# Optimization experiments

Measured on AMD Instinct MI355X. Metric: run time of the kernel, lower is better.

## Reference

```python
import jax, jax.numpy as jnp
import numpy as np

N = 4096
REG_STRENGTH = 1.0
BLOCK_EPS = 1e-6  # tolerance for detecting pooled-block boundaries in the backward


@jax.custom_vjp
def isotonic_l2(y):
    """argmin_{v_1 >= v_2 >= ... >= v_n} 0.5 * ||v - y||^2 (PAV solution).

    Computed via the exact minimax characterization, fully vectorized:
        v_i = min_{j <= i} max_{k >= i} mean(y[j..k])
    """
    return _iso_solution(y)


def _iso_solution(y):
    n = y.shape[0]
    cs = jnp.concatenate([jnp.zeros((1,), y.dtype), jnp.cumsum(y)])  # [n+1]
    idx = jnp.arange(n)
    j = idx[:, None]  # block start
    k = idx[None, :]  # block end
    length = (k - j + 1).astype(y.dtype)
    A = (cs[k + 1] - cs[j]) / length            # mean(y[j..k]) where k >= j
    A = jnp.where(k >= j, A, -jnp.inf)
    # M[j, i] = max_{k >= i} A[j, k]  (reverse cumulative max along k)
    M = jnp.flip(jax.lax.cummax(jnp.flip(A, axis=1), axis=1), axis=1)
    # v_i = min_{j <= i} M[j, i]  (cumulative min along j, take diagonal)
    v = jnp.diagonal(jax.lax.cummin(M, axis=0))
    return v


def _iso_fwd(y):
    v = _iso_solution(y)
    return v, v


def _iso_bwd(v, g):
    # Jacobian of PAV: within each pooled block, grad is the block mean of g.
    n = v.shape[0]
    drop = (v[:-1] - v[1:]) > BLOCK_EPS * jnp.maximum(jnp.abs(v[:-1]), 1.0)
    bid = jnp.concatenate([jnp.zeros((1,), jnp.int32),
                           jnp.cumsum(drop.astype(jnp.int32))])
    sums = jax.ops.segment_sum(g, bid, num_segments=n)
    cnts = jax.ops.segment_sum(jnp.ones_like(g), bid, num_segments=n)
    return ((sums / jnp.maximum(cnts, 1.0))[bid],)


isotonic_l2.defvjp(_iso_fwd, _iso_bwd)


def soft_rank(x, regularization_strength):
    """torchsort-style L2 soft rank: project x/eps onto permutahedron P([n..1])."""
    n = x.shape[0]
    theta = x / regularization_strength
    perm = jnp.argsort(-theta)          # descending sort permutation (constant wrt grad)
    s = theta[perm]
    w = jnp.arange(n, 0, -1, dtype=x.dtype)  # [n, n-1, ..., 1]
    sol = isotonic_l2(s - w)
    ranks_sorted = s - sol
    inv = jnp.argsort(perm)
    return ranks_sorted[inv]


def setup_inputs() -> dict:
    key = jax.random.key(0)
    kp, kt = jax.random.split(key)
    pred = jax.random.normal(kp, (N,), dtype=jnp.float32)
    target = jax.random.normal(kt, (N,), dtype=jnp.float32)
    return {"pred": pred, "target": target}


def reference(pred, target):
    p = soft_rank(pred, REG_STRENGTH)
    t = soft_rank(target, REG_STRENGTH)
    p = p - p.mean()
    p = p / jnp.linalg.norm(p)
    t = t - t.mean()
    t = t / jnp.linalg.norm(t)
    return 1.0 - jnp.sum(p * t)
```

## Files before the change

kernel.cpp:

```cpp
#include <hip/hip_runtime.h>
#include <math.h>

#define NEL   4096
#define NT    1024
#define HALF  512
#define EPT   8
#define CPT   4
#define CB    256

#define IX(p) ((p) + ((p) >> 3))

#define WSYNC() asm volatile("s_waitcnt lgkmcnt(0)" ::: "memory")

__global__ __launch_bounds__(CB)
void count_kernel(const float* __restrict__ pred,
                  const float* __restrict__ target,
                  unsigned int* __restrict__ counts) {
  __shared__ float jv[CB];
  const int arr = blockIdx.z;
  const float* __restrict__ x = arr ? target : pred;
  const int i     = blockIdx.x * CB + threadIdx.x;
  const int jbase = blockIdx.y * CB;

  jv[threadIdx.x] = x[jbase + threadIdx.x];
  const float xi = x[i];
  __syncthreads();

  const float4* jv4 = (const float4*)jv;
  unsigned int c = 0;
#pragma unroll 4
  for (int t4 = 0; t4 < CB / 4; t4++) {
    const float4 v = jv4[t4];
    const int j = jbase + 4 * t4;
    c += (v.x > xi || (v.x == xi && j + 0 < i)) ? 1u : 0u;
    c += (v.y > xi || (v.y == xi && j + 1 < i)) ? 1u : 0u;
    c += (v.z > xi || (v.z == xi && j + 2 < i)) ? 1u : 0u;
    c += (v.w > xi || (v.w == xi && j + 3 < i)) ? 1u : 0u;
  }
  atomicAdd(&counts[arr * NEL + i], c);
}

__device__ inline void pav_merge(double* P, int* C, const int lo, const int mid,
                                 const int hi) {
  const int llen = C[mid - 1];
  int cs = mid - llen;
  const int rlen = C[mid];
  int ce = mid + rlen - 1;
  const double Pmid = P[IX(mid)];
  double Pcs = P[IX(cs)], Pce1 = P[IX(ce + 1)];
  if ((Pmid - Pcs) * (double)rlen <= (Pce1 - Pmid) * (double)llen) {
    bool changed = true;
    while (changed) {
      changed = false;
      while (cs > lo) {
        const int l2 = C[cs - 1];
        const double Pl = P[IX(cs - l2)];
        if ((Pcs - Pl) * (double)(ce - cs + 1) <= (Pce1 - Pcs) * (double)l2) {
          cs -= l2; Pcs = Pl; changed = true;
        } else break;
      }
      while (ce < hi - 1) {
        const int l2 = C[ce + 1];
        const double Pr = P[IX(ce + 1 + l2)];
        if ((Pr - Pce1) * (double)(ce - cs + 1) >= (Pce1 - Pcs) * (double)l2) {
          ce += l2; Pce1 = Pr; changed = true;
        } else break;
      }
    }
    const int len = ce - cs + 1;
    C[cs] = len;
    C[ce] = len;
  }
}

__global__ __launch_bounds__(NT)
void pav_loss_kernel(const float* __restrict__ pred,
                     const float* __restrict__ target,
                     const unsigned int* __restrict__ counts,
                     float* __restrict__ loss_out) {
  __shared__ float  s_val[2][IX(NEL - 1) + 2];
  __shared__ double s_P[2][IX(NEL) + 1];
  __shared__ int    s_cnt[2][NEL];
  __shared__ double s_wsum[2][HALF / 64];
  __shared__ int    s_nb[2];
  __shared__ double s_red[NT / 64][5];

  const int tid  = threadIdx.x;
  const int lane = tid & 63;
  const int wid  = tid >> 6;

  int rp[CPT], rt[CPT];
  {
    const uint4 a = ((const uint4*)counts)[tid];
    const uint4 b = ((const uint4*)counts)[NEL / 4 + tid];
    rp[0] = (int)a.x; rp[1] = (int)a.y; rp[2] = (int)a.z; rp[3] = (int)a.w;
    rt[0] = (int)b.x; rt[1] = (int)b.y; rt[2] = (int)b.z; rt[3] = (int)b.w;
    const float4 xp = ((const float4*)pred)[tid];
    const float4 xt = ((const float4*)target)[tid];
    s_val[0][IX(rp[0])] = xp.x; s_val[0][IX(rp[1])] = xp.y;
    s_val[0][IX(rp[2])] = xp.z; s_val[0][IX(rp[3])] = xp.w;
    s_val[1][IX(rt[0])] = xt.x; s_val[1][IX(rt[1])] = xt.y;
    s_val[1][IX(rt[2])] = xt.z; s_val[1][IX(rt[3])] = xt.w;
  }
  __syncthreads();

  const int arr = tid >> 9;
  const int tA  = tid & (HALF - 1);
  const int wA  = tA >> 6;
  const int b0  = tA * EPT;
  double* P = s_P[arr];
  int*    C = s_cnt[arr];

  double c[EPT];
  {
    double acc = 0.0;
#pragma unroll
    for (int e = 0; e < EPT; e++) {
      const int p = b0 + e;
      acc += (double)s_val[arr][IX(p)] - (double)(NEL - p);
      c[e] = acc;
    }
  }
  const double tot = c[EPT - 1];
  double sc = tot;
#pragma unroll
  for (int d = 1; d < 64; d <<= 1) {
    const double o = __shfl_up(sc, d, 64);
    if (lane >= d) sc += o;
  }
  if (lane == 63) s_wsum[arr][wA] = sc;
  __syncthreads();
  double wexcl = 0.0;
#pragma unroll
  for (int w = 0; w < HALF / 64; w++)
    wexcl += (w < wA) ? s_wsum[arr][w] : 0.0;
  const double excl = wexcl + (sc - tot);
#pragma unroll
  for (int e = 0; e < EPT; e++) P[IX(b0 + 1 + e)] = excl + c[e];
  if (lane == 0) P[IX(b0)] = excl;

  double nmx[EPT]; int dmx[EPT];
  double vn[EPT];  int vd[EPT];
  {
#pragma unroll
    for (int j = 0; j < EPT; j++) {
      nmx[j] = c[7] - (j ? c[j - 1] : 0.0);
      dmx[j] = EPT - j;
    }
    double mn = nmx[0]; int md = dmx[0];
#pragma unroll
    for (int j = 1; j < EPT; j++)
      if (nmx[j] * (double)md < mn * (double)dmx[j]) { mn = nmx[j]; md = dmx[j]; }
    vn[7] = mn; vd[7] = md;
#pragma unroll
    for (int p = EPT - 2; p >= 0; p--) {
#pragma unroll
      for (int j = 0; j < EPT - 1; j++) {
        if (j <= p) {
          const double cnum = c[p] - (j ? c[j - 1] : 0.0);
          const int cden = p - j + 1;
          if (cnum * (double)dmx[j] > nmx[j] * (double)cden) {
            nmx[j] = cnum; dmx[j] = cden;
          }
        }
      }
      double mn2 = nmx[0]; int md2 = dmx[0];
#pragma unroll
      for (int j = 1; j < EPT - 1; j++) {
        if (j <= p) {
          if (nmx[j] * (double)md2 < mn2 * (double)dmx[j]) {
            mn2 = nmx[j]; md2 = dmx[j];
          }
        }
      }
      vn[p] = mn2; vd[p] = md2;
    }
  }
  {
    int runstart = b0;
#pragma unroll
    for (int e = 1; e < EPT; e++) {
      const bool neq = (vd[e] != vd[e - 1]) ||
                       (__double_as_longlong(vn[e]) !=
                        __double_as_longlong(vn[e - 1]));
      if (neq) {
        const int len = b0 + e - runstart;
        C[runstart] = len;
        C[b0 + e - 1] = len;
        runstart = b0 + e;
      }
    }
    const int len = b0 + EPT - runstart;
    C[runstart] = len;
    C[b0 + EPT - 1] = len;
  }
  WSYNC();

  const int wbase = wA * 512;
#pragma unroll
  for (int m = EPT; m <= 256; m <<= 1) {
    const int nm = 512 / (2 * m);
    if (lane < nm) {
      const int lo = wbase + lane * 2 * m;
      pav_merge(P, C, lo, lo + m, lo + 2 * m);
    }
    WSYNC();
  }
  __syncthreads();

  if (wA == 0) {
#pragma unroll
    for (int m = 512; m <= 2048; m <<= 1) {
      const int nm = NEL / (2 * m);
      if (lane < nm) {
        const int lo = lane * 2 * m;
        pav_merge(P, C, lo, lo + m, lo + 2 * m);
      }
      WSYNC();
    }
    if (lane == 0) {
      int s = 0, b = 0;
      while (s < NEL) {
        const int cc = C[s];
        C[b] = s;
        b++;
        s += cc;
      }
      s_nb[arr] = b;
    }
  }
  __syncthreads();

  const int nb = s_nb[arr];
#pragma unroll
  for (int e = 0; e < EPT; e++) {
    const int p = b0 + e;
    int lo = 0, hi = nb - 1;
    while (lo < hi) {
      const int md = (lo + hi + 1) >> 1;
      if (C[md] <= p) lo = md; else hi = md - 1;
    }
    const int st = C[lo];
    const int en = (lo + 1 < nb) ? C[lo + 1] : NEL;
    const double v = (P[IX(en)] - P[IX(st)]) / (double)(en - st);
    s_val[arr][IX(p)] = (float)((double)s_val[arr][IX(p)] - v);
  }
  __syncthreads();

  double Sp = 0.0, Sq = 0.0, Spp = 0.0, Sqq = 0.0, Spq = 0.0;
#pragma unroll
  for (int e = 0; e < CPT; e++) {
    const double p = (double)s_val[0][IX(rp[e])];
    const double q = (double)s_val[1][IX(rt[e])];
    Sp += p; Sq += q; Spp += p * p; Sqq += q * q; Spq += p * q;
  }
#pragma unroll
  for (int d = 32; d > 0; d >>= 1) {
    Sp  += __shfl_down(Sp,  d, 64);
    Sq  += __shfl_down(Sq,  d, 64);
    Spp += __shfl_down(Spp, d, 64);
    Sqq += __shfl_down(Sqq, d, 64);
    Spq += __shfl_down(Spq, d, 64);
  }
  if (lane == 0) {
    s_red[wid][0] = Sp;  s_red[wid][1] = Sq;  s_red[wid][2] = Spp;
    s_red[wid][3] = Sqq; s_red[wid][4] = Spq;
  }
  __syncthreads();
  if (tid == 0) {
    double a0 = 0, a1 = 0, a2 = 0, a3 = 0, a4 = 0;
    for (int w = 0; w < NT / 64; w++) {
      a0 += s_red[w][0]; a1 += s_red[w][1]; a2 += s_red[w][2];
      a3 += s_red[w][3]; a4 += s_red[w][4];
    }
    const double n  = (double)NEL;
    const double mp = a0 / n, mq = a1 / n;
    const double cov = a4 - n * mp * mq;
    const double vp  = a2 - n * mp * mp;
    const double vq  = a3 - n * mq * mq;
    loss_out[0] = (float)(1.0 - cov / sqrt(vp * vq));
  }
}

extern "C" void kernel_launch(void* const* d_in, const int* in_sizes, int n_in,
                              void* d_out, int out_size, void* d_ws, size_t ws_size,
                              hipStream_t stream) {
  const float* pred   = (const float*)d_in[0];
  const float* target = (const float*)d_in[1];
  unsigned int* counts = (unsigned int*)d_ws;
  float* out = (float*)d_out;

  hipMemsetAsync(counts, 0, 2 * NEL * sizeof(unsigned int), stream);
  hipLaunchKernelGGL(count_kernel, dim3(NEL / CB, NEL / CB, 2), dim3(CB), 0,
                     stream, pred, target, counts);
  hipLaunchKernelGGL(pav_loss_kernel, dim3(1), dim3(NT), 0, stream,
                     pred, target, counts, out);
}
```

Before: 80.52 us.

## Drop memset and atomics in rank count; scatter sorted values from count kernel

The counting kernel now has each block load the whole array into shared memory, and four lanes split the comparisons for one element and combine their partial counts with shuffles. This removes the memset, the global atomics and the 2D grid. The count kernel also scatters each value to its sorted position in a workspace buffer, so the single-block PAV kernel reads sorted values directly instead of scattering them through shared memory behind a barrier. The trade-off is fewer, longer-running count blocks (128 instead of 512) and extra workspace use.

```diff
diff --git a/kernel.cpp b/kernel.cpp
--- a/kernel.cpp
+++ b/kernel.cpp
@@ -6,38 +6,50 @@
 #define HALF  512
 #define EPT   8
 #define CPT   4
-#define CB    256
+#define LPI   4
+#define QPAD  1032
 
 #define IX(p) ((p) + ((p) >> 3))
 
 #define WSYNC() asm volatile("s_waitcnt lgkmcnt(0)" ::: "memory")
 
-__global__ __launch_bounds__(CB)
+__global__ __launch_bounds__(256)
 void count_kernel(const float* __restrict__ pred,
                   const float* __restrict__ target,
-                  unsigned int* __restrict__ counts) {
-  __shared__ float jv[CB];
-  const int arr = blockIdx.z;
+                  unsigned int* __restrict__ counts,
+                  float* __restrict__ sortedv) {
+  __shared__ float jv[4 * QPAD];
+  const int arr = blockIdx.y;
   const float* __restrict__ x = arr ? target : pred;
-  const int i     = blockIdx.x * CB + threadIdx.x;
-  const int jbase = blockIdx.y * CB;
-
-  jv[threadIdx.x] = x[jbase + threadIdx.x];
-  const float xi = x[i];
-  __syncthreads();
-
-  const float4* jv4 = (const float4*)jv;
+  const int tid = threadIdx.x;
+  const int q   = tid & (LPI - 1);
+  const int i   = blockIdx.x * 64 + (tid >> 2);
+
+  {
+    const float4* x4 = (const float4*)x;
+    for (int w4 = tid; w4 < NEL / 4; w4 += 256) {
+      const int qq = w4 >> 8;
+      ((float4*)(jv + qq * QPAD))[w4 & 255] = x4[w4];
+    }
+  }
+  __syncthreads();
+
+  const float xi = jv[(i >> 10) * QPAD + (i & 1023)];
+  const float4* mv = (const float4*)(jv + q * QPAD);
   unsigned int c = 0;
-#pragma unroll 4
-  for (int t4 = 0; t4 < CB / 4; t4++) {
-    const float4 v = jv4[t4];
-    const int j = jbase + 4 * t4;
+#pragma unroll 8
+  for (int t4 = 0; t4 < 256; t4++) {
+    const float4 v = mv[t4];
+    const int j = q * 1024 + 4 * t4;
     c += (v.x > xi || (v.x == xi && j + 0 < i)) ? 1u : 0u;
     c += (v.y > xi || (v.y == xi && j + 1 < i)) ? 1u : 0u;
     c += (v.z > xi || (v.z == xi && j + 2 < i)) ? 1u : 0u;
     c += (v.w > xi || (v.w == xi && j + 3 < i)) ? 1u : 0u;
   }
-  atomicAdd(&counts[arr * NEL + i], c);
+  c += __shfl_xor((int)c, 1);
+  c += __shfl_xor((int)c, 2);
+  if (q == 0) counts[arr * NEL + i] = c;
+  if (q == 1) sortedv[arr * NEL + c] = xi;
 }
 
 __device__ inline void pav_merge(double* P, int* C, const int lo, const int mid,
@@ -74,11 +86,10 @@
 }
 
 __global__ __launch_bounds__(NT)
-void pav_loss_kernel(const float* __restrict__ pred,
-                     const float* __restrict__ target,
-                     const unsigned int* __restrict__ counts,
+void pav_loss_kernel(const unsigned int* __restrict__ counts,
+                     const float* __restrict__ sortedv,
                      float* __restrict__ loss_out) {
-  __shared__ float  s_val[2][IX(NEL - 1) + 2];
+  __shared__ float  s_rank[2][IX(NEL - 1) + 1];
   __shared__ double s_P[2][IX(NEL) + 1];
   __shared__ int    s_cnt[2][NEL];
   __shared__ double s_wsum[2][HALF / 64];
@@ -95,14 +106,7 @@
     const uint4 b = ((const uint4*)counts)[NEL / 4 + tid];
     rp[0] = (int)a.x; rp[1] = (int)a.y; rp[2] = (int)a.z; rp[3] = (int)a.w;
     rt[0] = (int)b.x; rt[1] = (int)b.y; rt[2] = (int)b.z; rt[3] = (int)b.w;
-    const float4 xp = ((const float4*)pred)[tid];
-    const float4 xt = ((const float4*)target)[tid];
-    s_val[0][IX(rp[0])] = xp.x; s_val[0][IX(rp[1])] = xp.y;
-    s_val[0][IX(rp[2])] = xp.z; s_val[0][IX(rp[3])] = xp.w;
-    s_val[1][IX(rt[0])] = xt.x; s_val[1][IX(rt[1])] = xt.y;
-    s_val[1][IX(rt[2])] = xt.z; s_val[1][IX(rt[3])] = xt.w;
-  }
-  __syncthreads();
+  }
 
   const int arr = tid >> 9;
   const int tA  = tid & (HALF - 1);
@@ -111,13 +115,20 @@
   double* P = s_P[arr];
   int*    C = s_cnt[arr];
 
+  float xv[EPT];
+  {
+    const float4 v0 = ((const float4*)sortedv)[arr * (NEL / 4) + 2 * tA];
+    const float4 v1 = ((const float4*)sortedv)[arr * (NEL / 4) + 2 * tA + 1];
+    xv[0] = v0.x; xv[1] = v0.y; xv[2] = v0.z; xv[3] = v0.w;
+    xv[4] = v1.x; xv[5] = v1.y; xv[6] = v1.z; xv[7] = v1.w;
+  }
+
   double c[EPT];
   {
     double acc = 0.0;
 #pragma unroll
     for (int e = 0; e < EPT; e++) {
-      const int p = b0 + e;
-      acc += (double)s_val[arr][IX(p)] - (double)(NEL - p);
+      acc += (double)xv[e] - (double)(NEL - (b0 + e));
       c[e] = acc;
     }
   }
@@ -243,15 +254,15 @@
     const int st = C[lo];
     const int en = (lo + 1 < nb) ? C[lo + 1] : NEL;
     const double v = (P[IX(en)] - P[IX(st)]) / (double)(en - st);
-    s_val[arr][IX(p)] = (float)((double)s_val[arr][IX(p)] - v);
+    s_rank[arr][IX(p)] = (float)((double)xv[e] - v);
   }
   __syncthreads();
 
   double Sp = 0.0, Sq = 0.0, Spp = 0.0, Sqq = 0.0, Spq = 0.0;
 #pragma unroll
   for (int e = 0; e < CPT; e++) {
-    const double p = (double)s_val[0][IX(rp[e])];
-    const double q = (double)s_val[1][IX(rt[e])];
+    const double p = (double)s_rank[0][IX(rp[e])];
+    const double q = (double)s_rank[1][IX(rt[e])];
     Sp += p; Sq += q; Spp += p * p; Sqq += q * q; Spq += p * q;
   }
 #pragma unroll
@@ -287,12 +298,12 @@
                               hipStream_t stream) {
   const float* pred   = (const float*)d_in[0];
   const float* target = (const float*)d_in[1];
-  unsigned int* counts = (unsigned int*)d_ws;
+  unsigned int* counts  = (unsigned int*)d_ws;
+  float*        sortedv = (float*)((char*)d_ws + 2 * NEL * sizeof(unsigned int));
   float* out = (float*)d_out;
 
-  hipMemsetAsync(counts, 0, 2 * NEL * sizeof(unsigned int), stream);
-  hipLaunchKernelGGL(count_kernel, dim3(NEL / CB, NEL / CB, 2), dim3(CB), 0,
-                     stream, pred, target, counts);
+  hipLaunchKernelGGL(count_kernel, dim3(64, 2), dim3(256), 0, stream,
+                     pred, target, counts, sortedv);
   hipLaunchKernelGGL(pav_loss_kernel, dim3(1), dim3(NT), 0, stream,
-                     pred, target, counts, out);
+                     counts, sortedv, out);
 }
```

New measurement: 102.1 us. 1.27x slower.

## Halve PAV block threads, 16 elements each, with sequential stack-based local PAV

Applied to the files above, without the earlier changes.

Drops the PAV kernel from 1024 to 512 threads, each handling 16 sorted elements instead of 8. The unrolled minimax computation of each thread's local isotonic solution is replaced by a sequential pool-adjacent-violators loop over shared-memory prefix sums and block lengths. The in-wave merge tree now starts at 16 and covers 1024 elements per wave, so a single wave does fewer cross-wave merge levels. The trade-off is fewer threads sharing the work, a longer serial per-thread loop, and more shared-memory traffic in the local pass.

```diff
diff --git a/kernel.cpp b/kernel.cpp
--- a/kernel.cpp
+++ b/kernel.cpp
@@ -2,10 +2,10 @@
 #include <math.h>
 
 #define NEL   4096
-#define NT    1024
-#define HALF  512
-#define EPT   8
-#define CPT   4
+#define NT    512
+#define HALF  256
+#define EPT   16
+#define CPT   8
 #define CB    256
 
 #define IX(p) ((p) + ((p) >> 3))
@@ -91,20 +91,30 @@
 
   int rp[CPT], rt[CPT];
   {
-    const uint4 a = ((const uint4*)counts)[tid];
-    const uint4 b = ((const uint4*)counts)[NEL / 4 + tid];
-    rp[0] = (int)a.x; rp[1] = (int)a.y; rp[2] = (int)a.z; rp[3] = (int)a.w;
-    rt[0] = (int)b.x; rt[1] = (int)b.y; rt[2] = (int)b.z; rt[3] = (int)b.w;
-    const float4 xp = ((const float4*)pred)[tid];
-    const float4 xt = ((const float4*)target)[tid];
-    s_val[0][IX(rp[0])] = xp.x; s_val[0][IX(rp[1])] = xp.y;
-    s_val[0][IX(rp[2])] = xp.z; s_val[0][IX(rp[3])] = xp.w;
-    s_val[1][IX(rt[0])] = xt.x; s_val[1][IX(rt[1])] = xt.y;
-    s_val[1][IX(rt[2])] = xt.z; s_val[1][IX(rt[3])] = xt.w;
-  }
-  __syncthreads();
-
-  const int arr = tid >> 9;
+    const uint4 a0 = ((const uint4*)counts)[2 * tid];
+    const uint4 a1 = ((const uint4*)counts)[2 * tid + 1];
+    const uint4 b0_ = ((const uint4*)counts)[NEL / 4 + 2 * tid];
+    const uint4 b1_ = ((const uint4*)counts)[NEL / 4 + 2 * tid + 1];
+    rp[0] = (int)a0.x; rp[1] = (int)a0.y; rp[2] = (int)a0.z; rp[3] = (int)a0.w;
+    rp[4] = (int)a1.x; rp[5] = (int)a1.y; rp[6] = (int)a1.z; rp[7] = (int)a1.w;
+    rt[0] = (int)b0_.x; rt[1] = (int)b0_.y; rt[2] = (int)b0_.z; rt[3] = (int)b0_.w;
+    rt[4] = (int)b1_.x; rt[5] = (int)b1_.y; rt[6] = (int)b1_.z; rt[7] = (int)b1_.w;
+    const float4 xp0 = ((const float4*)pred)[2 * tid];
+    const float4 xp1 = ((const float4*)pred)[2 * tid + 1];
+    const float4 xt0 = ((const float4*)target)[2 * tid];
+    const float4 xt1 = ((const float4*)target)[2 * tid + 1];
+    s_val[0][IX(rp[0])] = xp0.x; s_val[0][IX(rp[1])] = xp0.y;
+    s_val[0][IX(rp[2])] = xp0.z; s_val[0][IX(rp[3])] = xp0.w;
+    s_val[0][IX(rp[4])] = xp1.x; s_val[0][IX(rp[5])] = xp1.y;
+    s_val[0][IX(rp[6])] = xp1.z; s_val[0][IX(rp[7])] = xp1.w;
+    s_val[1][IX(rt[0])] = xt0.x; s_val[1][IX(rt[1])] = xt0.y;
+    s_val[1][IX(rt[2])] = xt0.z; s_val[1][IX(rt[3])] = xt0.w;
+    s_val[1][IX(rt[4])] = xt1.x; s_val[1][IX(rt[5])] = xt1.y;
+    s_val[1][IX(rt[6])] = xt1.z; s_val[1][IX(rt[7])] = xt1.w;
+  }
+  __syncthreads();
+
+  const int arr = tid >> 8;
   const int tA  = tid & (HALF - 1);
   const int wA  = tA >> 6;
   const int b0  = tA * EPT;
@@ -139,67 +149,28 @@
   for (int e = 0; e < EPT; e++) P[IX(b0 + 1 + e)] = excl + c[e];
   if (lane == 0) P[IX(b0)] = excl;
 
-  double nmx[EPT]; int dmx[EPT];
-  double vn[EPT];  int vd[EPT];
-  {
-#pragma unroll
-    for (int j = 0; j < EPT; j++) {
-      nmx[j] = c[7] - (j ? c[j - 1] : 0.0);
-      dmx[j] = EPT - j;
-    }
-    double mn = nmx[0]; int md = dmx[0];
-#pragma unroll
-    for (int j = 1; j < EPT; j++)
-      if (nmx[j] * (double)md < mn * (double)dmx[j]) { mn = nmx[j]; md = dmx[j]; }
-    vn[7] = mn; vd[7] = md;
-#pragma unroll
-    for (int p = EPT - 2; p >= 0; p--) {
-#pragma unroll
-      for (int j = 0; j < EPT - 1; j++) {
-        if (j <= p) {
-          const double cnum = c[p] - (j ? c[j - 1] : 0.0);
-          const int cden = p - j + 1;
-          if (cnum * (double)dmx[j] > nmx[j] * (double)cden) {
-            nmx[j] = cnum; dmx[j] = cden;
-          }
-        }
-      }
-      double mn2 = nmx[0]; int md2 = dmx[0];
-#pragma unroll
-      for (int j = 1; j < EPT - 1; j++) {
-        if (j <= p) {
-          if (nmx[j] * (double)md2 < mn2 * (double)dmx[j]) {
-            mn2 = nmx[j]; md2 = dmx[j];
-          }
-        }
-      }
-      vn[p] = mn2; vd[p] = md2;
-    }
-  }
-  {
-    int runstart = b0;
-#pragma unroll
-    for (int e = 1; e < EPT; e++) {
-      const bool neq = (vd[e] != vd[e - 1]) ||
-                       (__double_as_longlong(vn[e]) !=
-                        __double_as_longlong(vn[e - 1]));
-      if (neq) {
-        const int len = b0 + e - runstart;
-        C[runstart] = len;
-        C[b0 + e - 1] = len;
-        runstart = b0 + e;
-      }
-    }
-    const int len = b0 + EPT - runstart;
-    C[runstart] = len;
-    C[b0 + EPT - 1] = len;
+  C[b0] = 1;
+  for (int p = b0 + 1; p < b0 + EPT; p++) {
+    int cs = p;
+    const double Pe = P[IX(p + 1)];
+    while (cs > b0) {
+      const int l2 = C[cs - 1];
+      const int lb = cs - l2;
+      const double Pcs = P[IX(cs)];
+      const double Plb = (lb == b0) ? excl : P[IX(lb)];
+      if ((Pcs - Plb) * (double)(p - cs + 1) <= (Pe - Pcs) * (double)l2)
+        cs = lb;
+      else break;
+    }
+    C[cs] = p - cs + 1;
+    C[p]  = p - cs + 1;
   }
   WSYNC();
 
-  const int wbase = wA * 512;
-#pragma unroll
-  for (int m = EPT; m <= 256; m <<= 1) {
-    const int nm = 512 / (2 * m);
+  const int wbase = wA * 1024;
+#pragma unroll
+  for (int m = EPT; m <= 512; m <<= 1) {
+    const int nm = 1024 / (2 * m);
     if (lane < nm) {
       const int lo = wbase + lane * 2 * m;
       pav_merge(P, C, lo, lo + m, lo + 2 * m);
@@ -210,7 +181,7 @@
 
   if (wA == 0) {
 #pragma unroll
-    for (int m = 512; m <= 2048; m <<= 1) {
+    for (int m = 1024; m <= 2048; m <<= 1) {
       const int nm = NEL / (2 * m);
       if (lane < nm) {
         const int lo = lane * 2 * m;
```

Result: no change. 80.81 us (+0.4%).
